# Kernel tuning notes

Measured on AMD Instinct MI355X. Metric: run time of the kernel, lower is better.

Reference implementation:

```python
import jax, jax.numpy as jnp
import numpy as np

HID, H, D, DFF = 128, 4, 128, 2048   # hidden_dim, nheads, out_feats per head, dim_feedforward
N, E, B = 32768, 524288, 32
EPS = 1e-5
SLOPE = 0.2  # DGL EdgeGATConv negative_slope default


def setup_inputs() -> dict:
    key = jax.random.key(0)
    ks = jax.random.split(key, 16)
    s = 0.05
    return {
        "h": jax.random.normal(ks[0], (N, HID), jnp.float32),
        "e": jax.random.normal(ks[1], (E, 1), jnp.float32),
        "src": jax.random.randint(ks[2], (E,), 0, N, jnp.int32),
        "dst": jax.random.randint(ks[3], (E,), 0, N, jnp.int32),
        "batch_size": B,
        # EdgeGATConv params (fc / fc_edge / res_fc are bias-free in DGL)
        "W_fc": jax.random.normal(ks[4], (HID, H * D), jnp.float32) * s,
        "attn_l": jax.random.normal(ks[5], (H, D), jnp.float32) * s,
        "attn_r": jax.random.normal(ks[6], (H, D), jnp.float32) * s,
        "W_fe": jax.random.normal(ks[7], (1, H * D), jnp.float32) * s,
        "attn_e": jax.random.normal(ks[8], (H, D), jnp.float32) * s,
        "W_res": jax.random.normal(ks[9], (HID, H * D), jnp.float32) * s,
        "gat_bias": jnp.zeros((H * D,), jnp.float32),
        # linear_mha + norms + FFN
        "W_mha": jax.random.normal(ks[10], (H * D, HID), jnp.float32) * s,
        "b_mha": jnp.zeros((HID,), jnp.float32),
        "n1_g": jnp.ones((HID,), jnp.float32),
        "n1_b": jnp.zeros((HID,), jnp.float32),
        "n2_g": jnp.ones((HID,), jnp.float32),
        "n2_b": jnp.zeros((HID,), jnp.float32),
        "W1": jax.random.normal(ks[11], (HID, DFF), jnp.float32) * s,
        "b1": jnp.zeros((DFF,), jnp.float32),
        "W2": jax.random.normal(ks[12], (DFF, HID), jnp.float32) * s,
        "b2": jnp.zeros((HID,), jnp.float32),
    }


def _ln(x, g, b):
    mu = x.mean(-1, keepdims=True)
    var = ((x - mu) ** 2).mean(-1, keepdims=True)
    return (x - mu) * jax.lax.rsqrt(var + EPS) * g + b


def reference(h, e, src, dst, batch_size, W_fc, attn_l, attn_r, W_fe, attn_e,
              W_res, gat_bias, W_mha, b_mha, n1_g, n1_b, n2_g, n2_b,
              W1, b1, W2, b2):
    n = h.shape[0]
    h0 = h
    # --- EdgeGATConv (eval mode: dropouts are identity) ---
    ft = (h @ W_fc).reshape(n, H, D)                         # (N,H,D)
    el = jnp.einsum("nhd,hd->nh", ft, attn_l)                # (N,H)
    er = jnp.einsum("nhd,hd->nh", ft, attn_r)
    fe = (e @ W_fe).reshape(-1, H, D)                        # (E,H,D)
    ee = jnp.einsum("ehd,hd->eh", fe, attn_e)                # (E,H)
    sc = jax.nn.leaky_relu(el[src] + er[dst] + ee, SLOPE)    # (E,H)
    # segment softmax over incoming edges of each dst node
    m = jax.ops.segment_max(sc, dst, num_segments=n)         # (N,H)
    m = jnp.where(jnp.isfinite(m), m, 0.0)                   # empty segments
    w = jnp.exp(sc - m[dst])
    z = jax.ops.segment_sum(w, dst, num_segments=n)
    zd = z[dst]
    alpha = w / jnp.where(zd == 0, 1.0, zd)                  # (E,H)
    msg = ft[src] * alpha[:, :, None]                        # (E,H,D)
    rst = jax.ops.segment_sum(msg, dst, num_segments=n)      # (N,H,D)
    rst = rst + (h0 @ W_res).reshape(n, H, D) + gat_bias.reshape(1, H, D)
    # --- transformer wrapper ---
    x = jax.nn.relu(rst).reshape(n, H * D)
    x = jax.nn.relu(x @ W_mha + b_mha)
    x = _ln(h0 + x, n1_g, n1_b)
    x = x.reshape(batch_size, -1, x.shape[1])                # (B, N/B, HID)
    ff = jax.nn.relu(x @ W1 + b1) @ W2 + b2
    return _ln(x + ff, n2_g, n2_b)
```

## Files before the change

kernel.cpp:

```cpp
#include <hip/hip_runtime.h>
#include <hip/hip_bf16.h>
#include <hip/hip_fp16.h>

#define N_NODES 32768
#define E_EDGES 524288
#define HIDDIM 128
#define FDIM 512
#define DFF 2048
#define LN_EPS 1e-5f
#define SLOPE 0.2f
#define CAP 64

typedef __bf16 bf16_t;
typedef __bf16 bf16x8 __attribute__((ext_vector_type(8)));
typedef float f32x4 __attribute__((ext_vector_type(4)));
typedef float f32x2 __attribute__((ext_vector_type(2)));

#define GLD_LDS16(gp, lp) __builtin_amdgcn_global_load_lds( \
    (const __attribute__((address_space(1))) unsigned int*)(gp), \
    (__attribute__((address_space(3))) unsigned int*)(lp), 16, 0, 0)

__device__ inline unsigned char f32_to_e4m3(float v) {
#if __has_builtin(__builtin_amdgcn_cvt_pk_fp8_f32)
    return (unsigned char)(__builtin_amdgcn_cvt_pk_fp8_f32(v, v, 0, false) & 0xff);
#else
    unsigned bits = __float_as_uint(v);
    unsigned sign = (bits >> 24) & 0x80;
    float av = fabsf(v);
    if (av >= 448.f) return (unsigned char)(sign | 0x7E);
    int e = (int)((bits >> 23) & 0xFF) - 127;
    if (e < -6) { int n = (int)rintf(av * 512.f); return (unsigned char)(sign | n); }
    float ulp = exp2f((float)(e - 3));
    int n = (int)rintf(av / ulp);
    if (n == 16) { e += 1; n = 8; }
    return (unsigned char)(sign | ((e + 7) << 3) | (n - 8));
#endif
}
template<bool HI>
__device__ inline f32x2 e4m3x2_to_f32(unsigned u) {
#if __has_builtin(__builtin_amdgcn_cvt_pk_f32_fp8)
    return __builtin_amdgcn_cvt_pk_f32_fp8(u, HI);
#else
    f32x2 r;
    unsigned b0 = HI ? ((u >> 16) & 0xff) : (u & 0xff);
    unsigned b1 = HI ? ((u >> 24) & 0xff) : ((u >> 8) & 0xff);
    unsigned bs[2] = {b0, b1};
    for (int i = 0; i < 2; ++i) {
        unsigned b = bs[i];
        float s = (b & 0x80) ? -1.f : 1.f;
        int e = (b >> 3) & 15, m = b & 7;
        float v = e ? (8 + m) * exp2f((float)(e - 10)) : m * exp2f(-9.f);
        r[i] = s * v;
    }
    return r;
#endif
}

__device__ inline void pack_range(const float* __restrict__ B, bf16_t* __restrict__ out,
                                  int id, int N) {
    const int g = id / N, n = id % N;
    union { bf16_t b[8]; uint4 u; } pk;
#pragma unroll
    for (int j = 0; j < 8; ++j) pk.b[j] = (bf16_t)B[(size_t)(g * 8 + j) * N + n];
    *(uint4*)(out + (size_t)id * 8) = pk.u;
}

__global__ __launch_bounds__(256) void prep_kernel(const float* __restrict__ h, bf16_t* __restrict__ hb,
                                                   const float* __restrict__ W_fc, bf16_t* __restrict__ Wfc_p,
                                                   const float* __restrict__ W_res, bf16_t* __restrict__ Wres_p,
                                                   const float* __restrict__ W_mha, bf16_t* __restrict__ Wmha_p,
                                                   const float* __restrict__ W1, bf16_t* __restrict__ W1_p,
                                                   const float* __restrict__ W2, bf16_t* __restrict__ W2_p,
                                                   const float* __restrict__ W_fe, const float* __restrict__ attn_e,
                                                   float* __restrict__ ce) {
    int bid = blockIdx.x;
    const int tid = threadIdx.x;
    if (bid < 4096) {
        const int id = bid * 256 + tid;
        const float4 v = ((const float4*)h)[id];
        union { bf16_t b[4]; uint2 u; } pk;
        pk.b[0] = (bf16_t)v.x; pk.b[1] = (bf16_t)v.y; pk.b[2] = (bf16_t)v.z; pk.b[3] = (bf16_t)v.w;
        *(uint2*)(hb + (size_t)id * 4) = pk.u;
        return;
    }
    bid -= 4096;
    if (bid < 32)  { pack_range(W_fc,  Wfc_p,  bid * 256 + tid, 512);  return; }
    bid -= 32;
    if (bid < 32)  { pack_range(W_res, Wres_p, bid * 256 + tid, 512);  return; }
    bid -= 32;
    if (bid < 32)  { pack_range(W_mha, Wmha_p, bid * 256 + tid, 128);  return; }
    bid -= 32;
    if (bid < 128) { pack_range(W1,    W1_p,   bid * 256 + tid, 2048); return; }
    bid -= 128;
    if (bid < 128) { pack_range(W2,    W2_p,   bid * 256 + tid, 128);  return; }
    if (tid < 128) {
        const float4 w = ((const float4*)W_fe)[tid];
        const float4 a = ((const float4*)attn_e)[tid];
        float p = w.x * a.x + w.y * a.y + w.z * a.z + w.w * a.w;
        for (int off = 16; off; off >>= 1) p += __shfl_down(p, off, 32);
        if ((tid & 31) == 0) ce[tid >> 5] = p;
    }
}

__global__ __launch_bounds__(256, 2) void gemm_ftres(const bf16_t* __restrict__ A,
                                                     const bf16_t* __restrict__ Bf,
                                                     const bf16_t* __restrict__ Brs,
                                                     const float* __restrict__ attn_l,
                                                     const float* __restrict__ attn_r,
                                                     unsigned char* __restrict__ ft8,
                                                     float* __restrict__ el,
                                                     float* __restrict__ er,
                                                     bf16_t* __restrict__ res) {
    __shared__ __align__(16) bf16_t lA[4096];
    __shared__ __align__(16) bf16_t lBf[4096];
    __shared__ __align__(16) bf16_t lBr[4096];
    __shared__ float s_el[2][128], s_er[2][128];
    const int tid = threadIdx.x, lane = tid & 63, wave = tid >> 6;
    const int wm = (wave >> 1) * 64, wn = (wave & 1) * 64;
    const int row0 = blockIdx.y * 128;
    const int head = blockIdx.x, col0 = head * 128;
    const int ko = lane >> 4, rl = lane & 15;
    f32x4 accf[4][4] = {};
    f32x4 accr[4][4] = {};
    const int c0 = tid, c1 = tid + 256;
    const int g0 = c0 >> 7, m0 = c0 & 127;
    const int g1 = c1 >> 7, m1 = c1 & 127;
    for (int k0 = 0; k0 < 128; k0 += 32) {
        __syncthreads();
        GLD_LDS16(A + (size_t)(row0 + m0) * 128 + k0 + g0 * 8, lA + c0 * 8);
        GLD_LDS16(A + (size_t)(row0 + m1) * 128 + k0 + g1 * 8, lA + c1 * 8);
        GLD_LDS16(Bf + ((size_t)(k0 / 8 + g0) * 512 + col0 + m0) * 8, lBf + c0 * 8);
        GLD_LDS16(Bf + ((size_t)(k0 / 8 + g1) * 512 + col0 + m1) * 8, lBf + c1 * 8);
        GLD_LDS16(Brs + ((size_t)(k0 / 8 + g0) * 512 + col0 + m0) * 8, lBr + c0 * 8);
        GLD_LDS16(Brs + ((size_t)(k0 / 8 + g1) * 512 + col0 + m1) * 8, lBr + c1 * 8);
        __syncthreads();
        bf16x8 af[4], bff[4], bfr[4];
#pragma unroll
        for (int i = 0; i < 4; ++i) {
            af[i]  = *(const bf16x8*)&lA[(ko * 128 + wm + i * 16 + rl) * 8];
            bff[i] = *(const bf16x8*)&lBf[(ko * 128 + wn + i * 16 + rl) * 8];
            bfr[i] = *(const bf16x8*)&lBr[(ko * 128 + wn + i * 16 + rl) * 8];
        }
#pragma unroll
        for (int i = 0; i < 4; ++i)
#pragma unroll
            for (int j = 0; j < 4; ++j) {
                accf[i][j] = __builtin_amdgcn_mfma_f32_16x16x32_bf16(af[i], bff[j], accf[i][j], 0, 0, 0);
                accr[i][j] = __builtin_amdgcn_mfma_f32_16x16x32_bf16(af[i], bfr[j], accr[i][j], 0, 0, 0);
            }
    }
    const int cr = (lane >> 4) * 4, cc = lane & 15;
    float al[4], ar[4];
#pragma unroll
    for (int j = 0; j < 4; ++j) {
        al[j] = attn_l[col0 + wn + j * 16 + cc];
        ar[j] = attn_r[col0 + wn + j * 16 + cc];
    }
#pragma unroll
    for (int i = 0; i < 4; ++i)
#pragma unroll
        for (int r = 0; r < 4; ++r) {
            const int row = row0 + wm + i * 16 + cr + r;
            float pel = 0.f, per = 0.f;
#pragma unroll
            for (int j = 0; j < 4; ++j) {
                const int col = col0 + wn + j * 16 + cc;
                const float v = accf[i][j][r];
                ft8[(size_t)row * 512 + col] = f32_to_e4m3(v);
                res[(size_t)row * 512 + col] = (bf16_t)accr[i][j][r];
                pel += v * al[j];
                per += v * ar[j];
            }
#pragma unroll
            for (int m = 1; m < 16; m <<= 1) {
                pel += __shfl_xor(pel, m);
                per += __shfl_xor(per, m);
            }
            if (cc == 0) {
                s_el[wn >> 6][wm + i * 16 + cr + r] = pel;
                s_er[wn >> 6][wm + i * 16 + cr + r] = per;
            }
        }
    __syncthreads();
    if (tid < 128) {
        el[(size_t)(row0 + tid) * 4 + head] = s_el[0][tid] + s_el[1][tid];
        er[(size_t)(row0 + tid) * 4 + head] = s_er[0][tid] + s_er[1][tid];
    }
}

__global__ __launch_bounds__(512, 2) void ffn_mega(const bf16_t* __restrict__ x1,
                                                   const bf16_t* __restrict__ Wm,
                                                   const float* __restrict__ b_mha,
                                                   const float* __restrict__ h0,
                                                   const float* __restrict__ n1g,
                                                   const float* __restrict__ n1b,
                                                   const bf16_t* __restrict__ W1p,
                                                   const float* __restrict__ b1,
                                                   const bf16_t* __restrict__ W2p,
                                                   const float* __restrict__ b2,
                                                   const float* __restrict__ gamma,
                                                   const float* __restrict__ beta,
                                                   float* __restrict__ out) {
    __shared__ __align__(16) bf16_t lW1[3][8192];
    __shared__ __align__(16) bf16_t lW2[4][8192];
    __shared__ __align__(16) bf16_t lY[2][8192];
    __shared__ float s_s1[2][128], s_s2[2][128], s_mu[128], s_rs[128];
    const int tid = threadIdx.x, lane = tid & 63, wave = tid >> 6;
    const int kh  = wave & 1;
    const int ds  = wave & 3;
    const int cg  = (wave >> 1) & 1;
    const int rg  = wave >> 2;
    const int wr  = rg * 64;
    const int wc1 = ds * 16;
    const int wc2 = cg * 64;
    const int row0 = blockIdx.x * 128;
    const int ko = lane >> 4, rl = lane & 15;
    const int cr = ko * 4, cc = rl;

    {
        const int rg2 = wave >> 1;
        const int cg2 = wave & 1;
        const int gg = tid >> 7, mm = tid & 127;
        auto stage0 = [&](int s) {
            bf16_t* lab = &lW2[s & 3][0];
            GLD_LDS16(x1 + (size_t)(row0 + mm) * 512 + s * 32 + gg * 8, lab + tid * 8);
            GLD_LDS16(Wm + ((size_t)(s * 4 + gg) * 128 + mm) * 8, lab + 4096 + tid * 8);
        };
        f32x4 am[2][4] = {};
        stage0(0); stage0(1); stage0(2);
        for (int s = 0; s < 16; ++s) {
            __builtin_amdgcn_sched_barrier(0);
            if (s < 14)       asm volatile("s_waitcnt vmcnt(4)" ::: "memory");
            else if (s == 14) asm volatile("s_waitcnt vmcnt(2)" ::: "memory");
            else              asm volatile("s_waitcnt vmcnt(0)" ::: "memory");
            __builtin_amdgcn_s_barrier();
            __builtin_amdgcn_sched_barrier(0);
            if (s + 3 < 16) stage0(s + 3);
            const bf16_t* lab = &lW2[s & 3][0];
            bf16x8 af[2], bfm[4];
#pragma unroll
            for (int i = 0; i < 2; ++i)
                af[i] = *(const bf16x8*)&lab[(ko * 128 + rg2 * 32 + i * 16 + rl) * 8];
#pragma unroll
            for (int j = 0; j < 4; ++j)
                bfm[j] = *(const bf16x8*)&lab[4096 + (ko * 128 + cg2 * 64 + j * 16 + rl) * 8];
            __builtin_amdgcn_s_setprio(1);
#pragma unroll
            for (int i = 0; i < 2; ++i)
#pragma unroll
                for (int j = 0; j < 4; ++j)
                    am[i][j] = __builtin_amdgcn_mfma_f32_16x16x32_bf16(af[i], bfm[j], am[i][j], 0, 0, 0);
            __builtin_amdgcn_s_setprio(0);
        }
#pragma unroll
        for (int j = 0; j < 4; ++j) {
            const int col = cg2 * 64 + j * 16 + cc;
            const float bb = b_mha[col];
#pragma unroll
            for (int i = 0; i < 2; ++i)
#pragma unroll
                for (int r = 0; r < 4; ++r) {
                    const int row = row0 + rg2 * 32 + i * 16 + cr + r;
                    am[i][j][r] = fmaxf(am[i][j][r] + bb, 0.f) + h0[(size_t)row * 128 + col];
                }
        }
#pragma unroll
        for (int i = 0; i < 2; ++i)
#pragma unroll
            for (int r = 0; r < 4; ++r) {
                float s1 = 0.f, s2 = 0.f;
#pragma unroll
                for (int j = 0; j < 4; ++j) { const float v = am[i][j][r]; s1 += v; s2 += v * v; }
#pragma unroll
                for (int m = 1; m < 16; m <<= 1) {
                    s1 += __shfl_xor(s1, m);
                    s2 += __shfl_xor(s2, m);
                }
                if (cc == 0) {
                    s_s1[cg2][rg2 * 32 + i * 16 + cr + r] = s1;
                    s_s2[cg2][rg2 * 32 + i * 16 + cr + r] = s2;
                }
            }
        __syncthreads();
        if (tid < 128) {
            const float a = s_s1[0][tid] + s_s1[1][tid];
            const float q = s_s2[0][tid] + s_s2[1][tid];
            const float mu = a * (1.f / 128.f);
            s_mu[tid] = mu;
            s_rs[tid] = rsqrtf(q * (1.f / 128.f) - mu * mu + LN_EPS);
        }
        __syncthreads();
        bf16_t* lX0 = &lW1[0][0];
#pragma unroll
        for (int j = 0; j < 4; ++j) {
            const int col = cg2 * 64 + j * 16 + cc;
            const float gg2 = n1g[col], bbta = n1b[col];
#pragma unroll
            for (int i = 0; i < 2; ++i)
#pragma unroll
                for (int r = 0; r < 4; ++r) {
                    const int rloc = rg2 * 32 + i * 16 + cr + r;
                    lX0[((col >> 3) * 128 + rloc) * 8 + (col & 7)] =
                        (bf16_t)((am[i][j][r] - s_mu[rloc]) * s_rs[rloc] * gg2 + bbta);
                }
        }
    }
    __syncthreads();

    bf16_t* lX = &lW1[0][0];
    bf16x8 afx[4][4];
#pragma unroll
    for (int ir = 0; ir < 4; ++ir)
#pragma unroll
        for (int kk = 0; kk < 4; ++kk)
            afx[ir][kk] = *(const bf16x8*)&lX[((kk * 4 + ko) * 128 + wr + ir * 16 + rl) * 8];
    unsigned x3p[32];
    if (!kh) {
#pragma unroll
        for (int ir = 0; ir < 4; ++ir)
#pragma unroll
            for (int j = 0; j < 4; ++j)
#pragma unroll
                for (int rr = 0; rr < 2; ++rr) {
                    const int col = wc2 + j * 16 + cc;
                    const int rw = wr + ir * 16 + cr + rr * 2;
                    const unsigned short a = *(const unsigned short*)&lX[((col >> 3) * 128 + rw) * 8 + (col & 7)];
                    const unsigned short b = *(const unsigned short*)&lX[((col >> 3) * 128 + rw + 1) * 8 + (col & 7)];
                    x3p[ir * 8 + j * 2 + rr] = (unsigned)a | ((unsigned)b << 16);
                }
    }
    asm volatile("s_waitcnt lgkmcnt(0)" ::: "memory");
    __builtin_amdgcn_s_barrier();
    __builtin_amdgcn_sched_barrier(0);

    auto stage_chunk = [&](int chn, bf16_t* w1d, bf16_t* w2d) {
#pragma unroll
        for (int it = 0; it < 2; ++it) {
            const int c = it * 512 + tid, g = c >> 6, n = c & 63;
            GLD_LDS16(W1p + ((size_t)g * 2048 + chn * 64 + n) * 8, w1d + c * 8);
        }
#pragma unroll
        for (int it = 0; it < 2; ++it) {
            const int c = it * 512 + tid, g = c >> 7, n = c & 127;
            GLD_LDS16(W2p + ((size_t)(chn * 8 + g) * 128 + n) * 8, w2d + c * 8);
        }
    };

    f32x4 xacc[4][4] = {};

    auto gemm1 = [&](int chn, const bf16_t* w1c, bf16_t* ydst) {
        f32x4 yacc[4] = {};
        __builtin_amdgcn_s_setprio(1);
#pragma unroll
        for (int kk = 0; kk < 4; ++kk) {
            const bf16x8 bw = *(const bf16x8*)&w1c[((kk * 4 + ko) * 64 + wc1 + rl) * 8];
#pragma unroll
            for (int ir = 0; ir < 4; ++ir)
                yacc[ir] = __builtin_amdgcn_mfma_f32_16x16x32_bf16(bw, afx[ir][kk], yacc[ir], 0, 0, 0);
        }
        __builtin_amdgcn_s_setprio(0);
        const int dffb = wc1 + cr;
        const float4 bb = *(const float4*)(b1 + chn * 64 + dffb);
#pragma unroll
        for (int ir = 0; ir < 4; ++ir) {
            const int rowx = wr + ir * 16 + cc;
            union { bf16_t b[4]; uint2 u; } pk;
            pk.b[0] = (bf16_t)fmaxf(yacc[ir][0] + bb.x, 0.f);
            pk.b[1] = (bf16_t)fmaxf(yacc[ir][1] + bb.y, 0.f);
            pk.b[2] = (bf16_t)fmaxf(yacc[ir][2] + bb.z, 0.f);
            pk.b[3] = (bf16_t)fmaxf(yacc[ir][3] + bb.w, 0.f);
            *(uint2*)&ydst[((dffb >> 3) * 128 + rowx) * 8 + (dffb & 7)] = pk.u;
        }
    };

    auto gemm2 = [&](const bf16_t* w2c, const bf16_t* ysrc) {
        bf16x8 ay[4], bw2[4];
#pragma unroll
        for (int ir = 0; ir < 4; ++ir)
            ay[ir] = *(const bf16x8*)&ysrc[((kh * 4 + ko) * 128 + wr + ir * 16 + rl) * 8];
#pragma unroll
        for (int j = 0; j < 4; ++j)
            bw2[j] = *(const bf16x8*)&w2c[((kh * 4 + ko) * 128 + wc2 + j * 16 + rl) * 8];
        __builtin_amdgcn_s_setprio(1);
#pragma unroll
        for (int ir = 0; ir < 4; ++ir)
#pragma unroll
            for (int j = 0; j < 4; ++j)
                xacc[ir][j] = __builtin_amdgcn_mfma_f32_16x16x32_bf16(ay[ir], bw2[j], xacc[ir][j], 0, 0, 0);
        __builtin_amdgcn_s_setprio(0);
    };

#pragma unroll
    for (int pc = 0; pc < 2; ++pc)
        stage_chunk(pc, lW1[pc], lW2[pc]);
    asm volatile("s_waitcnt vmcnt(4)" ::: "memory");
    __builtin_amdgcn_s_barrier();
    __builtin_amdgcn_sched_barrier(0);

    stage_chunk(2, lW1[2], lW2[2]);
    gemm1(0, lW1[0], lY[0]);
    __builtin_amdgcn_sched_barrier(0);
    asm volatile("s_waitcnt vmcnt(4) lgkmcnt(0)" ::: "memory");
    __builtin_amdgcn_s_barrier();
    __builtin_amdgcn_sched_barrier(0);

    int r1 = 1, sb1 = 0, r2 = 0, sb2 = 3, p = 1;
#pragma unroll 1
    for (int i = 1; i < 32; ++i) {
        if (i < 30)
            stage_chunk(i + 2, lW1[sb1], lW2[sb2]);
        gemm1(i, lW1[r1], lY[p]);
        gemm2(lW2[r2], lY[p ^ 1]);
        __builtin_amdgcn_sched_barrier(0);
        if (i < 30)
            asm volatile("s_waitcnt vmcnt(4) lgkmcnt(0)" ::: "memory");
        else if (i == 30)
            asm volatile("s_waitcnt vmcnt(2) lgkmcnt(0)" ::: "memory");
        else
            asm volatile("s_waitcnt vmcnt(0) lgkmcnt(0)" ::: "memory");
        __builtin_amdgcn_s_barrier();
        __builtin_amdgcn_sched_barrier(0);
        r1 = (r1 == 2) ? 0 : r1 + 1;
        sb1 = (sb1 == 2) ? 0 : sb1 + 1;
        r2 = (r2 == 3) ? 0 : r2 + 1;
        sb2 = (sb2 == 3) ? 0 : sb2 + 1;
        p ^= 1;
    }
    gemm2(lW2[3], lY[1]);

    __syncthreads();
    {
        const int q = (wave >> 1) & 3;
        float* scr = (q < 2) ? ((float*)&lW1[0][0] + q * 4352)
                             : ((float*)&lW2[0][0] + (q - 2) * 4352);
        if (kh) {
#pragma unroll
            for (int ir = 0; ir < 4; ++ir)
#pragma unroll
                for (int j = 0; j < 4; ++j)
                    *(f32x4*)(scr + lane * 68 + (ir * 4 + j) * 4) = xacc[ir][j];
        }
        __syncthreads();
        if (!kh) {
#pragma unroll
            for (int ir = 0; ir < 4; ++ir)
#pragma unroll
                for (int j = 0; j < 4; ++j)
                    xacc[ir][j] += *(const f32x4*)(scr + lane * 68 + (ir * 4 + j) * 4);
        }
    }

    if (!kh) {
#pragma unroll
        for (int j = 0; j < 4; ++j) {
            const int col = wc2 + j * 16 + cc;
            const float bb = b2[col];
#pragma unroll
            for (int ir = 0; ir < 4; ++ir)
#pragma unroll
                for (int r = 0; r < 4; ++r) {
                    const unsigned dw = x3p[ir * 8 + j * 2 + (r >> 1)];
                    const float xv = __uint_as_float((r & 1) ? (dw & 0xFFFF0000u) : (dw << 16));
                    xacc[ir][j][r] += bb + xv;
                }
        }
#pragma unroll
        for (int ir = 0; ir < 4; ++ir)
#pragma unroll
            for (int r = 0; r < 4; ++r) {
                float s1v = 0.f, s2v = 0.f;
#pragma unroll
                for (int j = 0; j < 4; ++j) { const float v = xacc[ir][j][r]; s1v += v; s2v += v * v; }
#pragma unroll
                for (int m = 1; m < 16; m <<= 1) {
                    s1v += __shfl_xor(s1v, m);
                    s2v += __shfl_xor(s2v, m);
                }
                if (cc == 0) {
                    s_s1[cg][wr + ir * 16 + cr + r] = s1v;
                    s_s2[cg][wr + ir * 16 + cr + r] = s2v;
                }
            }
    }
    __syncthreads();
    if (tid < 128) {
        const float a = s_s1[0][tid] + s_s1[1][tid];
        const float q = s_s2[0][tid] + s_s2[1][tid];
        const float mu = a * (1.f / 128.f);
        s_mu[tid] = mu;
        s_rs[tid] = rsqrtf(q * (1.f / 128.f) - mu * mu + LN_EPS);
    }
    __syncthreads();
    if (!kh) {
#pragma unroll
        for (int j = 0; j < 4; ++j) {
            const int col = wc2 + j * 16 + cc;
            const float gg = gamma[col], bb = beta[col];
#pragma unroll
            for (int ir = 0; ir < 4; ++ir)
#pragma unroll
                for (int r = 0; r < 4; ++r) {
                    const int rloc = wr + ir * 16 + cr + r;
                    out[(size_t)(row0 + rloc) * 128 + col] =
                        (xacc[ir][j][r] - s_mu[rloc]) * s_rs[rloc] * gg + bb;
                }
        }
    }
}

__global__ __launch_bounds__(256) void edge_build(const float* __restrict__ evals,
                                                  const int* __restrict__ src,
                                                  const int* __restrict__ dst,
                                                  const float* __restrict__ el,
                                                  const float* __restrict__ er,
                                                  const float* __restrict__ ce,
                                                  int* __restrict__ cursor,
                                                  uint4* __restrict__ csr) {
    const int e = blockIdx.x * 256 + threadIdx.x;
    const int s = src[e], d = dst[e];
    const float ev = evals[e];
    const float4 l = *(const float4*)(el + (size_t)s * 4);
    const float4 r = *(const float4*)(er + (size_t)d * 4);
    const float4 c = *(const float4*)ce;
    float4 w;
    {
        float v;
        v = l.x + r.x + ev * c.x; v = v >= 0.f ? v : SLOPE * v; w.x = __expf(v);
        v = l.y + r.y + ev * c.y; v = v >= 0.f ? v : SLOPE * v; w.y = __expf(v);
        v = l.z + r.z + ev * c.z; v = v >= 0.f ? v : SLOPE * v; w.z = __expf(v);
        v = l.w + r.w + ev * c.w; v = v >= 0.f ? v : SLOPE * v; w.w = __expf(v);
    }
    const int pos = atomicAdd(&cursor[d], 1);
    if (pos < CAP) {
        uint4 rec;
        rec.x = (unsigned)__half_as_ushort(__float2half(w.x)) |
                ((unsigned)__half_as_ushort(__float2half(w.y)) << 16);
        rec.y = (unsigned)__half_as_ushort(__float2half(w.z)) |
                ((unsigned)__half_as_ushort(__float2half(w.w)) << 16);
        rec.z = (unsigned)s;
        rec.w = 0u;
        csr[(size_t)d * CAP + pos] = rec;
    }
}

__device__ inline float w_of(const uint4& rec, int ht) {
    const unsigned pair = (ht < 2) ? rec.x : rec.y;
    const unsigned sh = (ht & 1) ? (pair >> 16) : (pair & 0xffffu);
    return __half2float(__ushort_as_half((unsigned short)sh));
}

__global__ __launch_bounds__(128) void aggregate_kernel(const unsigned char* __restrict__ ft8,
                                                        const bf16_t* __restrict__ res,
                                                        const int* __restrict__ cursor,
                                                        const uint4* __restrict__ csr,
                                                        const float* __restrict__ gat_bias,
                                                        bf16_t* __restrict__ x1) {
    const int n = blockIdx.x, t = threadIdx.x;
    __shared__ uint4 s_rec[CAP];
    const int deg = min(cursor[n], CAP);
    const int ht = t >> 5;
    if (t < deg) s_rec[t] = csr[(size_t)n * CAP + t];
    __syncthreads();
    float4 acc = {0.f, 0.f, 0.f, 0.f};
    float z = 0.f;
    int j = 0;
    for (; j + 8 <= deg; j += 8) {
        unsigned u[8];
        float w[8];
#pragma unroll
        for (int q = 0; q < 8; ++q) {
            const uint4 rc = s_rec[j + q];
            w[q] = w_of(rc, ht);
            u[q] = *(const unsigned*)(ft8 + (size_t)rc.z * 512 + t * 4);
        }
#pragma unroll
        for (int q = 0; q < 8; ++q) {
            z += w[q];
            const f32x2 lo = e4m3x2_to_f32<false>(u[q]), hi = e4m3x2_to_f32<true>(u[q]);
            acc.x += w[q] * lo[0]; acc.y += w[q] * lo[1];
            acc.z += w[q] * hi[0]; acc.w += w[q] * hi[1];
        }
    }
    for (; j < deg; ++j) {
        const uint4 rc = s_rec[j];
        const float w = w_of(rc, ht);
        z += w;
        const unsigned u = *(const unsigned*)(ft8 + (size_t)rc.z * 512 + t * 4);
        const f32x2 lo = e4m3x2_to_f32<false>(u);
        const f32x2 hi = e4m3x2_to_f32<true>(u);
        acc.x += w * lo[0]; acc.y += w * lo[1];
        acc.z += w * hi[0]; acc.w += w * hi[1];
    }
    const float rz = deg > 0 ? 1.f / z : 0.f;
    const uint2 ur = *(const uint2*)(res + (size_t)n * FDIM + t * 4);
    const float4 gb = ((const float4*)gat_bias)[t];
    union { bf16_t b[4]; uint2 u; } pk;
    pk.b[0] = (bf16_t)fmaxf(acc.x * rz + __uint_as_float(ur.x << 16) + gb.x, 0.f);
    pk.b[1] = (bf16_t)fmaxf(acc.y * rz + __uint_as_float(ur.x & 0xFFFF0000u) + gb.y, 0.f);
    pk.b[2] = (bf16_t)fmaxf(acc.z * rz + __uint_as_float(ur.y << 16) + gb.z, 0.f);
    pk.b[3] = (bf16_t)fmaxf(acc.w * rz + __uint_as_float(ur.y & 0xFFFF0000u) + gb.w, 0.f);
    *(uint2*)(x1 + (size_t)n * FDIM + t * 4) = pk.u;
}

extern "C" void kernel_launch(void* const* d_in, const int* in_sizes, int n_in,
                              void* d_out, int out_size, void* d_ws, size_t ws_size,
                              hipStream_t stream) {
    const float* h        = (const float*)d_in[0];
    const float* evals    = (const float*)d_in[1];
    const int*   src      = (const int*)d_in[2];
    const int*   dst      = (const int*)d_in[3];
    const float* W_fc     = (const float*)d_in[5];
    const float* attn_l   = (const float*)d_in[6];
    const float* attn_r   = (const float*)d_in[7];
    const float* W_fe     = (const float*)d_in[8];
    const float* attn_e   = (const float*)d_in[9];
    const float* W_res    = (const float*)d_in[10];
    const float* gat_bias = (const float*)d_in[11];
    const float* W_mha    = (const float*)d_in[12];
    const float* b_mha    = (const float*)d_in[13];
    const float* n1_g     = (const float*)d_in[14];
    const float* n1_b     = (const float*)d_in[15];
    const float* n2_g     = (const float*)d_in[16];
    const float* n2_b     = (const float*)d_in[17];
    const float* W1       = (const float*)d_in[18];
    const float* b1       = (const float*)d_in[19];
    const float* W2       = (const float*)d_in[20];
    const float* b2       = (const float*)d_in[21];

    char* ws = (char*)d_ws;
    unsigned char* ft8 = (unsigned char*)(ws + 0);
    bf16_t* res     = (bf16_t*)(ws + 16777216ull);
    bf16_t* x1      = (bf16_t*)(ws + 50331648ull);
    uint4*  csr     = (uint4*) (ws + 83886080ull);
    bf16_t* hb      = (bf16_t*)(ws + 134217728ull);
    bf16_t* Wfc_p   = (bf16_t*)(ws + 142606336ull);
    bf16_t* Wres_p  = (bf16_t*)(ws + 142737408ull);
    bf16_t* Wmha_p  = (bf16_t*)(ws + 142868480ull);
    bf16_t* W1_p    = (bf16_t*)(ws + 142999552ull);
    bf16_t* W2_p    = (bf16_t*)(ws + 143523840ull);
    float*  el      = (float*) (ws + 144048128ull);
    float*  er      = (float*) (ws + 144572416ull);
    float*  ce      = (float*) (ws + 145096704ull);
    int*    cursor  = (int*)   (ws + 145096768ull);

    if (ws_size < 146000000ull) return;

    (void)hipMemsetAsync(cursor, 0, 131072, stream);

    prep_kernel<<<4449, 256, 0, stream>>>(h, hb, W_fc, Wfc_p, W_res, Wres_p,
                                          W_mha, Wmha_p, W1, W1_p, W2, W2_p,
                                          W_fe, attn_e, ce);
    gemm_ftres<<<dim3(4, 256), 256, 0, stream>>>(hb, Wfc_p, Wres_p, attn_l, attn_r, ft8, el, er, res);
    edge_build<<<E_EDGES / 256, 256, 0, stream>>>(evals, src, dst, el, er, ce, cursor, csr);
    aggregate_kernel<<<N_NODES, 128, 0, stream>>>(ft8, res, cursor, csr, gat_bias, x1);
    ffn_mega<<<256, 512, 0, stream>>>(x1, Wmha_p, b_mha, h, n1_g, n1_b,
                                      W1_p, b1, W2_p, b2, n2_g, n2_b, (float*)d_out);
}
```

Measured before the change: 270.9 us.

## Restructure FFN pipeline into 128-wide DFF chunks and unroll aggregate gathers by 16

The FFN mega-kernel's pipeline changes from 64-wide DFF chunks with triple/quad-buffered W1/W2 staging to 128-wide chunks. W1 is single-buffered and W2 double-buffered, and loads are interleaved between the gemm1 and gemm2 phases with two barriers per chunk. LDS is repacked: the LayerNorm scratch aliases the Y buffer and the reduction scratch moves into the W2 buffers. This halves the loop trip count and cuts per-iteration barrier overhead, at the cost of shallower prefetch (a full vmcnt(0) wait each half-step), which may expose load latency. Separately, the aggregate kernel gains a 16-wide gather loop so more independent loads are in flight per node.

```diff
diff --git a/kernel.cpp b/kernel.cpp
--- a/kernel.cpp
+++ b/kernel.cpp
@@ -201,17 +201,20 @@
                                                    const float* __restrict__ gamma,
                                                    const float* __restrict__ beta,
                                                    float* __restrict__ out) {
-    __shared__ __align__(16) bf16_t lW1[3][8192];
-    __shared__ __align__(16) bf16_t lW2[4][8192];
-    __shared__ __align__(16) bf16_t lY[2][8192];
-    __shared__ float s_s1[2][128], s_s2[2][128], s_mu[128], s_rs[128];
+    __shared__ __align__(16) bf16_t lW1[16384];
+    __shared__ __align__(16) bf16_t lW2[2][16384];
+    __shared__ __align__(16) bf16_t lY[16384];
+    float* s_s1 = (float*)&lY[0];
+    float* s_s2 = (float*)&lY[0] + 256;
+    float* s_mu = (float*)&lY[0] + 512;
+    float* s_rs = (float*)&lY[0] + 640;
     const int tid = threadIdx.x, lane = tid & 63, wave = tid >> 6;
     const int kh  = wave & 1;
-    const int ds  = wave & 3;
+    const int ds4 = wave & 3;
     const int cg  = (wave >> 1) & 1;
     const int rg  = wave >> 2;
     const int wr  = rg * 64;
-    const int wc1 = ds * 16;
+    const int wc1 = ds4 * 32;
     const int wc2 = cg * 64;
     const int row0 = blockIdx.x * 128;
     const int ko = lane >> 4, rl = lane & 15;
@@ -222,7 +225,7 @@
         const int cg2 = wave & 1;
         const int gg = tid >> 7, mm = tid & 127;
         auto stage0 = [&](int s) {
-            bf16_t* lab = &lW2[s & 3][0];
+            bf16_t* lab = (bf16_t*)lW2 + (s & 3) * 8192;
             GLD_LDS16(x1 + (size_t)(row0 + mm) * 512 + s * 32 + gg * 8, lab + tid * 8);
             GLD_LDS16(Wm + ((size_t)(s * 4 + gg) * 128 + mm) * 8, lab + 4096 + tid * 8);
         };
@@ -236,7 +239,7 @@
             __builtin_amdgcn_s_barrier();
             __builtin_amdgcn_sched_barrier(0);
             if (s + 3 < 16) stage0(s + 3);
-            const bf16_t* lab = &lW2[s & 3][0];
+            const bf16_t* lab = (const bf16_t*)lW2 + (s & 3) * 8192;
             bf16x8 af[2], bfm[4];
 #pragma unroll
             for (int i = 0; i < 2; ++i)
@@ -277,20 +280,19 @@
                     s2 += __shfl_xor(s2, m);
                 }
                 if (cc == 0) {
-                    s_s1[cg2][rg2 * 32 + i * 16 + cr + r] = s1;
-                    s_s2[cg2][rg2 * 32 + i * 16 + cr + r] = s2;
+                    s_s1[cg2 * 128 + rg2 * 32 + i * 16 + cr + r] = s1;
+                    s_s2[cg2 * 128 + rg2 * 32 + i * 16 + cr + r] = s2;
                 }
             }
         __syncthreads();
         if (tid < 128) {
-            const float a = s_s1[0][tid] + s_s1[1][tid];
-            const float q = s_s2[0][tid] + s_s2[1][tid];
+            const float a = s_s1[tid] + s_s1[128 + tid];
+            const float q = s_s2[tid] + s_s2[128 + tid];
             const float mu = a * (1.f / 128.f);
             s_mu[tid] = mu;
             s_rs[tid] = rsqrtf(q * (1.f / 128.f) - mu * mu + LN_EPS);
         }
         __syncthreads();
-        bf16_t* lX0 = &lW1[0][0];
 #pragma unroll
         for (int j = 0; j < 4; ++j) {
             const int col = cg2 * 64 + j * 16 + cc;
@@ -300,20 +302,19 @@
 #pragma unroll
                 for (int r = 0; r < 4; ++r) {
                     const int rloc = rg2 * 32 + i * 16 + cr + r;
-                    lX0[((col >> 3) * 128 + rloc) * 8 + (col & 7)] =
+                    lW1[((col >> 3) * 128 + rloc) * 8 + (col & 7)] =
                         (bf16_t)((am[i][j][r] - s_mu[rloc]) * s_rs[rloc] * gg2 + bbta);
                 }
         }
     }
     __syncthreads();
 
-    bf16_t* lX = &lW1[0][0];
     bf16x8 afx[4][4];
 #pragma unroll
     for (int ir = 0; ir < 4; ++ir)
 #pragma unroll
         for (int kk = 0; kk < 4; ++kk)
-            afx[ir][kk] = *(const bf16x8*)&lX[((kk * 4 + ko) * 128 + wr + ir * 16 + rl) * 8];
+            afx[ir][kk] = *(const bf16x8*)&lW1[((kk * 4 + ko) * 128 + wr + ir * 16 + rl) * 8];
     unsigned x3p[32];
     if (!kh) {
 #pragma unroll
@@ -324,8 +325,8 @@
                 for (int rr = 0; rr < 2; ++rr) {
                     const int col = wc2 + j * 16 + cc;
                     const int rw = wr + ir * 16 + cr + rr * 2;
-                    const unsigned short a = *(const unsigned short*)&lX[((col >> 3) * 128 + rw) * 8 + (col & 7)];
-                    const unsigned short b = *(const unsigned short*)&lX[((col >> 3) * 128 + rw + 1) * 8 + (col & 7)];
+                    const unsigned short a = *(const unsigned short*)&lW1[((col >> 3) * 128 + rw) * 8 + (col & 7)];
+                    const unsigned short b = *(const unsigned short*)&lW1[((col >> 3) * 128 + rw + 1) * 8 + (col & 7)];
                     x3p[ir * 8 + j * 2 + rr] = (unsigned)a | ((unsigned)b << 16);
                 }
     }
@@ -333,106 +334,108 @@
     __builtin_amdgcn_s_barrier();
     __builtin_amdgcn_sched_barrier(0);
 
-    auto stage_chunk = [&](int chn, bf16_t* w1d, bf16_t* w2d) {
-#pragma unroll
-        for (int it = 0; it < 2; ++it) {
-            const int c = it * 512 + tid, g = c >> 6, n = c & 63;
-            GLD_LDS16(W1p + ((size_t)g * 2048 + chn * 64 + n) * 8, w1d + c * 8);
-        }
-#pragma unroll
-        for (int it = 0; it < 2; ++it) {
+    auto stage_W1 = [&](int chn) {
+#pragma unroll
+        for (int it = 0; it < 4; ++it) {
             const int c = it * 512 + tid, g = c >> 7, n = c & 127;
-            GLD_LDS16(W2p + ((size_t)(chn * 8 + g) * 128 + n) * 8, w2d + c * 8);
+            GLD_LDS16(W1p + ((size_t)g * 2048 + chn * 128 + n) * 8, lW1 + c * 8);
         }
     };
+    auto stage_W2 = [&](int chn, bf16_t* w2d) {
+#pragma unroll
+        for (int it = 0; it < 4; ++it) {
+            const int c = it * 512 + tid, g = c >> 7, n = c & 127;
+            GLD_LDS16(W2p + ((size_t)(chn * 16 + g) * 128 + n) * 8, w2d + c * 8);
+        }
+    };
 
     f32x4 xacc[4][4] = {};
 
-    auto gemm1 = [&](int chn, const bf16_t* w1c, bf16_t* ydst) {
-        f32x4 yacc[4] = {};
+    auto gemm1 = [&](int chn) {
+        f32x4 yacc[4][2] = {};
         __builtin_amdgcn_s_setprio(1);
 #pragma unroll
         for (int kk = 0; kk < 4; ++kk) {
-            const bf16x8 bw = *(const bf16x8*)&w1c[((kk * 4 + ko) * 64 + wc1 + rl) * 8];
+            bf16x8 bw[2];
+#pragma unroll
+            for (int jd = 0; jd < 2; ++jd)
+                bw[jd] = *(const bf16x8*)&lW1[((kk * 4 + ko) * 128 + wc1 + jd * 16 + rl) * 8];
+#pragma unroll
+            for (int jd = 0; jd < 2; ++jd)
+#pragma unroll
+                for (int ir = 0; ir < 4; ++ir)
+                    yacc[ir][jd] = __builtin_amdgcn_mfma_f32_16x16x32_bf16(bw[jd], afx[ir][kk], yacc[ir][jd], 0, 0, 0);
+        }
+        __builtin_amdgcn_s_setprio(0);
+#pragma unroll
+        for (int jd = 0; jd < 2; ++jd) {
+            const int dffb = wc1 + jd * 16 + cr;
+            const float4 bb = *(const float4*)(b1 + chn * 128 + dffb);
+#pragma unroll
+            for (int ir = 0; ir < 4; ++ir) {
+                const int rowx = wr + ir * 16 + cc;
+                union { bf16_t b[4]; uint2 u; } pk;
+                pk.b[0] = (bf16_t)fmaxf(yacc[ir][jd][0] + bb.x, 0.f);
+                pk.b[1] = (bf16_t)fmaxf(yacc[ir][jd][1] + bb.y, 0.f);
+                pk.b[2] = (bf16_t)fmaxf(yacc[ir][jd][2] + bb.z, 0.f);
+                pk.b[3] = (bf16_t)fmaxf(yacc[ir][jd][3] + bb.w, 0.f);
+                *(uint2*)&lY[((dffb >> 3) * 128 + rowx) * 8 + (dffb & 7)] = pk.u;
+            }
+        }
+    };
+
+    auto gemm2 = [&](const bf16_t* w2c) {
+        bf16x8 ay[2][4], bw2[2][4];
+#pragma unroll
+        for (int ks = 0; ks < 2; ++ks) {
 #pragma unroll
             for (int ir = 0; ir < 4; ++ir)
-                yacc[ir] = __builtin_amdgcn_mfma_f32_16x16x32_bf16(bw, afx[ir][kk], yacc[ir], 0, 0, 0);
-        }
-        __builtin_amdgcn_s_setprio(0);
-        const int dffb = wc1 + cr;
-        const float4 bb = *(const float4*)(b1 + chn * 64 + dffb);
-#pragma unroll
-        for (int ir = 0; ir < 4; ++ir) {
-            const int rowx = wr + ir * 16 + cc;
-            union { bf16_t b[4]; uint2 u; } pk;
-            pk.b[0] = (bf16_t)fmaxf(yacc[ir][0] + bb.x, 0.f);
-            pk.b[1] = (bf16_t)fmaxf(yacc[ir][1] + bb.y, 0.f);
-            pk.b[2] = (bf16_t)fmaxf(yacc[ir][2] + bb.z, 0.f);
-            pk.b[3] = (bf16_t)fmaxf(yacc[ir][3] + bb.w, 0.f);
-            *(uint2*)&ydst[((dffb >> 3) * 128 + rowx) * 8 + (dffb & 7)] = pk.u;
-        }
-    };
-
-    auto gemm2 = [&](const bf16_t* w2c, const bf16_t* ysrc) {
-        bf16x8 ay[4], bw2[4];
-#pragma unroll
-        for (int ir = 0; ir < 4; ++ir)
-            ay[ir] = *(const bf16x8*)&ysrc[((kh * 4 + ko) * 128 + wr + ir * 16 + rl) * 8];
-#pragma unroll
-        for (int j = 0; j < 4; ++j)
-            bw2[j] = *(const bf16x8*)&w2c[((kh * 4 + ko) * 128 + wc2 + j * 16 + rl) * 8];
+                ay[ks][ir] = *(const bf16x8*)&lY[((kh * 8 + ks * 4 + ko) * 128 + wr + ir * 16 + rl) * 8];
+#pragma unroll
+            for (int j = 0; j < 4; ++j)
+                bw2[ks][j] = *(const bf16x8*)&w2c[((kh * 8 + ks * 4 + ko) * 128 + wc2 + j * 16 + rl) * 8];
+        }
         __builtin_amdgcn_s_setprio(1);
 #pragma unroll
-        for (int ir = 0; ir < 4; ++ir)
-#pragma unroll
-            for (int j = 0; j < 4; ++j)
-                xacc[ir][j] = __builtin_amdgcn_mfma_f32_16x16x32_bf16(ay[ir], bw2[j], xacc[ir][j], 0, 0, 0);
+        for (int ks = 0; ks < 2; ++ks)
+#pragma unroll
+            for (int ir = 0; ir < 4; ++ir)
+#pragma unroll
+                for (int j = 0; j < 4; ++j)
+                    xacc[ir][j] = __builtin_amdgcn_mfma_f32_16x16x32_bf16(ay[ks][ir], bw2[ks][j], xacc[ir][j], 0, 0, 0);
         __builtin_amdgcn_s_setprio(0);
     };
 
-#pragma unroll
-    for (int pc = 0; pc < 2; ++pc)
-        stage_chunk(pc, lW1[pc], lW2[pc]);
-    asm volatile("s_waitcnt vmcnt(4)" ::: "memory");
+    stage_W1(0);
+    stage_W2(0, lW2[0]);
+    asm volatile("s_waitcnt vmcnt(0)" ::: "memory");
     __builtin_amdgcn_s_barrier();
     __builtin_amdgcn_sched_barrier(0);
 
-    stage_chunk(2, lW1[2], lW2[2]);
-    gemm1(0, lW1[0], lY[0]);
-    __builtin_amdgcn_sched_barrier(0);
-    asm volatile("s_waitcnt vmcnt(4) lgkmcnt(0)" ::: "memory");
-    __builtin_amdgcn_s_barrier();
-    __builtin_amdgcn_sched_barrier(0);
-
-    int r1 = 1, sb1 = 0, r2 = 0, sb2 = 3, p = 1;
+    int cur = 0;
 #pragma unroll 1
-    for (int i = 1; i < 32; ++i) {
-        if (i < 30)
-            stage_chunk(i + 2, lW1[sb1], lW2[sb2]);
-        gemm1(i, lW1[r1], lY[p]);
-        gemm2(lW2[r2], lY[p ^ 1]);
+    for (int ch = 0; ch < 16; ++ch) {
+        if (ch + 1 < 16)
+            stage_W2(ch + 1, lW2[cur ^ 1]);
+        gemm1(ch);
         __builtin_amdgcn_sched_barrier(0);
-        if (i < 30)
-            asm volatile("s_waitcnt vmcnt(4) lgkmcnt(0)" ::: "memory");
-        else if (i == 30)
-            asm volatile("s_waitcnt vmcnt(2) lgkmcnt(0)" ::: "memory");
-        else
-            asm volatile("s_waitcnt vmcnt(0) lgkmcnt(0)" ::: "memory");
+        asm volatile("s_waitcnt lgkmcnt(0)" ::: "memory");
         __builtin_amdgcn_s_barrier();
         __builtin_amdgcn_sched_barrier(0);
-        r1 = (r1 == 2) ? 0 : r1 + 1;
-        sb1 = (sb1 == 2) ? 0 : sb1 + 1;
-        r2 = (r2 == 3) ? 0 : r2 + 1;
-        sb2 = (sb2 == 3) ? 0 : sb2 + 1;
-        p ^= 1;
-    }
-    gemm2(lW2[3], lY[1]);
-
-    __syncthreads();
+        if (ch + 1 < 16)
+            stage_W1(ch + 1);
+        gemm2(lW2[cur]);
+        __builtin_amdgcn_sched_barrier(0);
+        asm volatile("s_waitcnt vmcnt(0) lgkmcnt(0)" ::: "memory");
+        __builtin_amdgcn_s_barrier();
+        __builtin_amdgcn_sched_barrier(0);
+        cur ^= 1;
+    }
+
     {
         const int q = (wave >> 1) & 3;
-        float* scr = (q < 2) ? ((float*)&lW1[0][0] + q * 4352)
-                             : ((float*)&lW2[0][0] + (q - 2) * 4352);
+        float* scr = (q < 3) ? ((float*)&lW2[0][0] + q * 4352)
+                             : ((float*)&lW1[0]);
         if (kh) {
 #pragma unroll
             for (int ir = 0; ir < 4; ++ir)
@@ -449,6 +452,7 @@
                     xacc[ir][j] += *(const f32x4*)(scr + lane * 68 + (ir * 4 + j) * 4);
         }
     }
+    __syncthreads();
 
     if (!kh) {
 #pragma unroll
@@ -477,15 +481,15 @@
                     s2v += __shfl_xor(s2v, m);
                 }
                 if (cc == 0) {
-                    s_s1[cg][wr + ir * 16 + cr + r] = s1v;
-                    s_s2[cg][wr + ir * 16 + cr + r] = s2v;
+                    s_s1[cg * 128 + wr + ir * 16 + cr + r] = s1v;
+                    s_s2[cg * 128 + wr + ir * 16 + cr + r] = s2v;
                 }
             }
     }
     __syncthreads();
     if (tid < 128) {
-        const float a = s_s1[0][tid] + s_s1[1][tid];
-        const float q = s_s2[0][tid] + s_s2[1][tid];
+        const float a = s_s1[tid] + s_s1[128 + tid];
+        const float q = s_s2[tid] + s_s2[128 + tid];
         const float mu = a * (1.f / 128.f);
         s_mu[tid] = mu;
         s_rs[tid] = rsqrtf(q * (1.f / 128.f) - mu * mu + LN_EPS);
@@ -564,6 +568,23 @@
     float4 acc = {0.f, 0.f, 0.f, 0.f};
     float z = 0.f;
     int j = 0;
+    for (; j + 16 <= deg; j += 16) {
+        unsigned u[16];
+        float w[16];
+#pragma unroll
+        for (int q = 0; q < 16; ++q) {
+            const uint4 rc = s_rec[j + q];
+            w[q] = w_of(rc, ht);
+            u[q] = *(const unsigned*)(ft8 + (size_t)rc.z * 512 + t * 4);
+        }
+#pragma unroll
+        for (int q = 0; q < 16; ++q) {
+            z += w[q];
+            const f32x2 lo = e4m3x2_to_f32<false>(u[q]), hi = e4m3x2_to_f32<true>(u[q]);
+            acc.x += w[q] * lo[0]; acc.y += w[q] * lo[1];
+            acc.z += w[q] * hi[0]; acc.w += w[q] * hi[1];
+        }
+    }
     for (; j + 8 <= deg; j += 8) {
         unsigned u[8];
         float w[8];
```

Result: slower. 288.6 us (+6.5%).
